# Performance work log

Hardware: AMD Instinct MI355X
Metric: run time of the kernel (lower is better)

Reference implementation:

```python
import jax, jax.numpy as jnp
import numpy as np

META_HIDDEN = 32


def _meta_apply(t, mw1, mb1, mw2, mb2):
    # t: [..., 3] triples; meta MLP 3 -> META_HIDDEN -> 1 (ReLU)
    h = jax.nn.relu(jnp.einsum('...k,hk->...h', t, mw1) + mb1)
    return jnp.einsum('...h,h->...', h, mw2[0]) + mb2[0]


def _meta_update_layer(v_in, w, v_out, mw1, mb1, mw2, mb2):
    # v_in: [I] (batch-0 input activations), w: [O, I], v_out: [O] (batch-0 output activations)
    # Builds the triples [v_i, w_ij, v_j] for every (i, j) pair and runs one batched meta pass.
    t = jnp.stack([
        jnp.broadcast_to(v_in[None, :], w.shape),
        w,
        jnp.broadcast_to(v_out[:, None], w.shape),
    ], axis=-1)  # [O, I, 3]
    return _meta_apply(t, mw1, mb1, mw2, mb2)  # [O, I] new weights


def setup_inputs() -> dict:
    key = jax.random.key(0)
    ks = jax.random.split(key, 12)
    I, H1, H2, O, B = 1024, 2048, 2048, 1024, 32
    def lin(kw, fan_in, fan_out):
        s = 1.0 / np.sqrt(fan_in)
        return jax.random.uniform(kw, (fan_out, fan_in), jnp.float32, -s, s)
    x = jax.random.normal(ks[0], (B, I), jnp.float32)
    w1 = lin(ks[1], I, H1); b1 = jax.random.uniform(ks[2], (H1,), jnp.float32, -1/np.sqrt(I), 1/np.sqrt(I))
    w2 = lin(ks[3], H1, H2); b2 = jax.random.uniform(ks[4], (H2,), jnp.float32, -1/np.sqrt(H1), 1/np.sqrt(H1))
    w3 = lin(ks[5], H2, O); b3 = jax.random.uniform(ks[6], (O,), jnp.float32, -1/np.sqrt(H2), 1/np.sqrt(H2))
    # meta network 3 -> META_HIDDEN -> 1
    mw1 = lin(ks[7], 3, META_HIDDEN); mb1 = jax.random.uniform(ks[8], (META_HIDDEN,), jnp.float32, -1/np.sqrt(3), 1/np.sqrt(3))
    mw2 = lin(ks[9], META_HIDDEN, 1); mb2 = jax.random.uniform(ks[10], (1,), jnp.float32, -1/np.sqrt(META_HIDDEN), 1/np.sqrt(META_HIDDEN))
    return {"x": x, "w1": w1, "b1": b1, "w2": w2, "b2": b2, "w3": w3, "b3": b3,
            "mw1": mw1, "mb1": mb1, "mw2": mw2, "mb2": mb2}


def reference(x, w1, b1, w2, b2, w3, b3, mw1, mb1, mw2, mb2):
    # Main 3-layer MLP forward (ReLU after every layer, including the last, as in the source).
    a0 = x
    a1 = jax.nn.relu(a0 @ w1.T + b1)
    a2 = jax.nn.relu(a1 @ w2.T + b2)
    out = jax.nn.relu(a2 @ w3.T + b3)
    # Per-weight meta update: original code loops over every (input, output) neuron pair of
    # each fc weight and writes meta_weight([v_i, w_ij, v_j]) back into the weight.
    # Only batch row 0 of the activations is used (impulse[i].data[0, idx]).
    nw1 = _meta_update_layer(a0[0], w1, a1[0], mw1, mb1, mw2, mb2)
    nw2 = _meta_update_layer(a1[0], w2, a2[0], mw1, mb1, mw2, mb2)
    nw3 = _meta_update_layer(a2[0], w3, out[0], mw1, mb1, mw2, mb2)
    return out, nw1, nw2, nw3
```

## Files before the change

kernel.cpp:

```cpp
#include <hip/hip_runtime.h>

#define NT 256

typedef float f2 __attribute__((ext_vector_type(2)));

__device__ __forceinline__ void meta_body(
    int g,
    const float* __restrict__ w1, const float* __restrict__ w2, const float* __restrict__ w3,
    const float* __restrict__ a0, const float* __restrict__ a1, const float* __restrict__ a2,
    const float* __restrict__ a3,
    float* __restrict__ n1, float* __restrict__ n2, float* __restrict__ n3,
    const float* __restrict__ mw1, const float* __restrict__ mb1,
    const float* __restrict__ mw2, const float* __restrict__ mb2) {
  const int n1c = (2048 * 1024) / 8;
  const int n2c = (2048 * 2048) / 8;

  const float* W; const float* vin; const float* vout; float* nw;
  int sh, e;
  if (g < n1c)            { W = w1; vin = a0; vout = a1; nw = n1; sh = 10; e = g; }
  else if (g < n1c + n2c) { W = w2; vin = a1; vout = a2; nw = n2; sh = 11; e = g - n1c; }
  else                    { W = w3; vin = a2; vout = a3; nw = n3; sh = 11; e = g - n1c - n2c; }

  const int base = e << 3;
  const int o = base >> sh;
  const int i0 = base & ((1 << sh) - 1);

  f2 wv[4], vv[4];
  {
    float4 t0 = *reinterpret_cast<const float4*>(&W[base]);
    float4 t1 = *reinterpret_cast<const float4*>(&W[base + 4]);
    wv[0] = (f2){t0.x, t0.y}; wv[1] = (f2){t0.z, t0.w};
    wv[2] = (f2){t1.x, t1.y}; wv[3] = (f2){t1.z, t1.w};
    float4 u0 = *reinterpret_cast<const float4*>(&vin[i0]);
    float4 u1 = *reinterpret_cast<const float4*>(&vin[i0 + 4]);
    vv[0] = (f2){u0.x, u0.y}; vv[1] = (f2){u0.z, u0.w};
    vv[2] = (f2){u1.x, u1.y}; vv[3] = (f2){u1.z, u1.w};
  }
  const float vo = vout[o];
  const float c2 = mb2[0];

  float r[32];
  #pragma unroll
  for (int j = 0; j < 32; ++j)
    r[j] = fmaf(mw1[3 * j + 2], vo, mb1[j]);

  f2 acc[4];
  #pragma unroll
  for (int p = 0; p < 4; ++p) acc[p] = (f2){c2, c2};

  const f2 zero = (f2){0.f, 0.f};
  #pragma unroll
  for (int j = 0; j < 32; ++j) {
    const float aj = mw1[3 * j];
    const float bj = mw1[3 * j + 1];
    const float mj = mw2[j];
    const f2 a2v = (f2){aj, aj};
    const f2 b2v = (f2){bj, bj};
    const f2 m2v = (f2){mj, mj};
    const f2 r2v = (f2){r[j], r[j]};
    #pragma unroll
    for (int p = 0; p < 4; ++p) {
#if __has_builtin(__builtin_elementwise_fma) && __has_builtin(__builtin_elementwise_max)
      f2 q = __builtin_elementwise_fma(a2v, vv[p], r2v);
      f2 h = __builtin_elementwise_fma(b2v, wv[p], q);
      h = __builtin_elementwise_max(h, zero);
      acc[p] = __builtin_elementwise_fma(m2v, h, acc[p]);
#else
      f2 h;
      h.x = fmaxf(fmaf(bj, wv[p].x, fmaf(aj, vv[p].x, r[j])), 0.f);
      h.y = fmaxf(fmaf(bj, wv[p].y, fmaf(aj, vv[p].y, r[j])), 0.f);
      acc[p].x = fmaf(mj, h.x, acc[p].x);
      acc[p].y = fmaf(mj, h.y, acc[p].y);
#endif
    }
  }

  float4 o0 = make_float4(acc[0].x, acc[0].y, acc[1].x, acc[1].y);
  float4 o1 = make_float4(acc[2].x, acc[2].y, acc[3].x, acc[3].y);
  *reinterpret_cast<float4*>(&nw[base])     = o0;
  *reinterpret_cast<float4*>(&nw[base + 4]) = o1;
}

template<int KL>
__device__ __forceinline__ void gemm_body(
    int gbid, const float* __restrict__ A, const float* __restrict__ W,
    float* __restrict__ P, int K, int O,
    float* __restrict__ Wt, float* __restrict__ At) {
  constexpr int NG = KL / 4;
  constexpr int PM = NG - 1;
  const int tid = threadIdx.x;
  const int ks = gbid & 31;
  const int obase = (gbid >> 5) << 7;
  const int kbeg = ks * KL;

  #pragma unroll
  for (int t = 0; t < (128 * NG) / NT; ++t) {
    const int s = tid + t * NT;
    const int r = s / NG, p = s % NG;
    const float4 v = *reinterpret_cast<const float4*>(
        &W[(size_t)(obase + r) * K + kbeg + 4 * p]);
    *reinterpret_cast<float4*>(&Wt[r * KL + 4 * (p ^ (r & PM))]) = v;
  }
  #pragma unroll
  for (int t = 0; t < (32 * NG + NT - 1) / NT; ++t) {
    const int s = tid + t * NT;
    if ((32 * NG) % NT == 0 || s < 32 * NG) {
      const int r = s / NG, p = s % NG;
      *reinterpret_cast<float4*>(&At[r * KL + 4 * p]) =
          *reinterpret_cast<const float4*>(&A[(size_t)r * K + kbeg + 4 * p]);
    }
  }
  __syncthreads();

  const int to = tid & 31;
  const int b0 = (tid >> 5) << 2;
  float acc[4][4];
  #pragma unroll
  for (int i = 0; i < 4; ++i)
    #pragma unroll
    for (int j = 0; j < 4; ++j) acc[i][j] = 0.f;

  #pragma unroll
  for (int gq = 0; gq < NG; ++gq) {
    float4 av[4], wv[4];
    #pragma unroll
    for (int j = 0; j < 4; ++j)
      av[j] = *reinterpret_cast<const float4*>(&At[(b0 + j) * KL + 4 * gq]);
    const int c = 4 * (gq ^ (to & PM));
    #pragma unroll
    for (int i = 0; i < 4; ++i)
      wv[i] = *reinterpret_cast<const float4*>(&Wt[(to + 32 * i) * KL + c]);
    #pragma unroll
    for (int i = 0; i < 4; ++i) {
      #pragma unroll
      for (int j = 0; j < 4; ++j) {
        acc[i][j] = fmaf(wv[i].x, av[j].x, acc[i][j]);
        acc[i][j] = fmaf(wv[i].y, av[j].y, acc[i][j]);
        acc[i][j] = fmaf(wv[i].z, av[j].z, acc[i][j]);
        acc[i][j] = fmaf(wv[i].w, av[j].w, acc[i][j]);
      }
    }
  }

  #pragma unroll
  for (int i = 0; i < 4; ++i)
    #pragma unroll
    for (int j = 0; j < 4; ++j)
      P[(size_t)(ks * 32 + b0 + j) * O + obase + to + 32 * i] = acc[i][j];
}

template<int KL>
__global__ __launch_bounds__(NT) void combo(
    int nGemm,
    const float* __restrict__ A, const float* __restrict__ W,
    float* __restrict__ P, int K, int O,
    int gbase,
    const float* __restrict__ w1, const float* __restrict__ w2, const float* __restrict__ w3,
    const float* __restrict__ a0, const float* __restrict__ a1, const float* __restrict__ a2,
    const float* __restrict__ a3,
    float* __restrict__ n1, float* __restrict__ n2, float* __restrict__ n3,
    const float* __restrict__ mw1, const float* __restrict__ mb1,
    const float* __restrict__ mw2, const float* __restrict__ mb2) {
  __shared__ float Wt[128 * KL];
  __shared__ float At[32 * KL];
  const int bid = blockIdx.x;
  if (bid < nGemm) {
    gemm_body<KL>(bid, A, W, P, K, O, Wt, At);
  } else {
    const int g = gbase + (bid - nGemm) * NT + threadIdx.x;
    meta_body(g, w1, w2, w3, a0, a1, a2, a3, n1, n2, n3, mw1, mb1, mw2, mb2);
  }
}

__global__ __launch_bounds__(NT) void meta_only(
    int gbase,
    const float* __restrict__ w1, const float* __restrict__ w2, const float* __restrict__ w3,
    const float* __restrict__ a0, const float* __restrict__ a1, const float* __restrict__ a2,
    const float* __restrict__ a3,
    float* __restrict__ n1, float* __restrict__ n2, float* __restrict__ n3,
    const float* __restrict__ mw1, const float* __restrict__ mb1,
    const float* __restrict__ mw2, const float* __restrict__ mb2) {
  const int g = gbase + blockIdx.x * NT + threadIdx.x;
  meta_body(g, w1, w2, w3, a0, a1, a2, a3, n1, n2, n3, mw1, mb1, mw2, mb2);
}

template<int OSH>
__global__ __launch_bounds__(NT) void red32(
    const float* __restrict__ P, const float* __restrict__ bias,
    float* __restrict__ C) {
  const int e = blockIdx.x * NT + threadIdx.x;
  const int o = e & ((1 << OSH) - 1);
  float s = 0.f;
  #pragma unroll
  for (int ks = 0; ks < 32; ++ks)
    s += P[((size_t)ks << (5 + OSH)) + e];
  C[e] = fmaxf(s + bias[o], 0.f);
}

extern "C" void kernel_launch(void* const* d_in, const int* in_sizes, int n_in,
                              void* d_out, int out_size, void* d_ws, size_t ws_size,
                              hipStream_t stream) {
  const float* x   = (const float*)d_in[0];
  const float* w1  = (const float*)d_in[1];
  const float* b1  = (const float*)d_in[2];
  const float* w2  = (const float*)d_in[3];
  const float* b2  = (const float*)d_in[4];
  const float* w3  = (const float*)d_in[5];
  const float* b3  = (const float*)d_in[6];
  const float* mw1 = (const float*)d_in[7];
  const float* mb1 = (const float*)d_in[8];
  const float* mw2 = (const float*)d_in[9];
  const float* mb2 = (const float*)d_in[10];

  float* out = (float*)d_out;
  float* n1  = out + 32 * 1024;
  float* n2  = n1 + 2048 * 1024;
  float* n3  = n2 + 2048 * 2048;

  float* ws = (float*)d_ws;
  float* a1 = ws;
  float* a2 = ws + 65536;
  float* P  = ws + 131072;

  combo<32><<<512, NT, 0, stream>>>(512, x, w1, P, 1024, 2048,
      0, w1, w2, w3, x, a1, a2, out, n1, n2, n3, mw1, mb1, mw2, mb2);
  red32<11><<<(32 * 2048) / NT, NT, 0, stream>>>(P, b1, a1);
  combo<64><<<512 + 1024, NT, 0, stream>>>(512, a1, w2, P, 2048, 2048,
      0, w1, w2, w3, x, a1, a2, out, n1, n2, n3, mw1, mb1, mw2, mb2);
  red32<11><<<(32 * 2048) / NT, NT, 0, stream>>>(P, b2, a2);
  combo<64><<<256 + 2048, NT, 0, stream>>>(256, a2, w3, P, 2048, 1024,
      262144, w1, w2, w3, x, a1, a2, out, n1, n2, n3, mw1, mb1, mw2, mb2);
  red32<10><<<(32 * 1024) / NT, NT, 0, stream>>>(P, b3, out);
  meta_only<<<1024, NT, 0, stream>>>(786432, w1, w2, w3, x, a1, a2, out,
                                     n1, n2, n3, mw1, mb1, mw2, mb2);
}
```

Before: 59.89 us.

## Transpose activations and compute GEMM split-K without shared memory

Replaces the shared-memory tiled split-K GEMM with a register-heavy scheme. Each thread owns one output neuron and accumulates all 32 batch rows over a K slice, reading activations stored transposed ([K][32]) so that loads are wave-uniform broadcasts. This adds a transpose kernel for x and reduction kernels that emit transposed activations plus a compact row-0 vector for the meta pass. The partial-sum buffer is moved into the n3 output region before that region is overwritten. The change removes LDS staging and barriers, at the cost of 32 accumulators per thread and strided per-thread weight reads.

```diff
diff --git a/kernel.cpp b/kernel.cpp
--- a/kernel.cpp
+++ b/kernel.cpp
@@ -3,6 +3,33 @@
 #define NT 256
 
 typedef float f2 __attribute__((ext_vector_type(2)));
+
+__global__ __launch_bounds__(NT) void transp_x(const float* __restrict__ x,
+                                               float* __restrict__ xT) {
+  __shared__ float T[64][33];
+  const int k0 = blockIdx.x * 64;
+  const int t = threadIdx.x;
+  {
+    const int s = t * 8;
+    const int b = s >> 6;
+    const int c = s & 63;
+    float4 v0 = *(const float4*)&x[b * 1024 + k0 + c];
+    float4 v1 = *(const float4*)&x[b * 1024 + k0 + c + 4];
+    T[c + 0][b] = v0.x; T[c + 1][b] = v0.y; T[c + 2][b] = v0.z; T[c + 3][b] = v0.w;
+    T[c + 4][b] = v1.x; T[c + 5][b] = v1.y; T[c + 6][b] = v1.z; T[c + 7][b] = v1.w;
+  }
+  __syncthreads();
+  {
+    const int s = t * 8;
+    const int r = s >> 5;
+    const int b0 = s & 31;
+    float o[8];
+    #pragma unroll
+    for (int q = 0; q < 8; ++q) o[q] = T[r][b0 + q];
+    *(float4*)&xT[(k0 + r) * 32 + b0]     = make_float4(o[0], o[1], o[2], o[3]);
+    *(float4*)&xT[(k0 + r) * 32 + b0 + 4] = make_float4(o[4], o[5], o[6], o[7]);
+  }
+}
 
 __device__ __forceinline__ void meta_body(
     int g,
@@ -75,84 +102,52 @@
     }
   }
 
-  float4 o0 = make_float4(acc[0].x, acc[0].y, acc[1].x, acc[1].y);
-  float4 o1 = make_float4(acc[2].x, acc[2].y, acc[3].x, acc[3].y);
-  *reinterpret_cast<float4*>(&nw[base])     = o0;
-  *reinterpret_cast<float4*>(&nw[base + 4]) = o1;
-}
-
-template<int KL>
+  *reinterpret_cast<float4*>(&nw[base])     = make_float4(acc[0].x, acc[0].y, acc[1].x, acc[1].y);
+  *reinterpret_cast<float4*>(&nw[base + 4]) = make_float4(acc[2].x, acc[2].y, acc[3].x, acc[3].y);
+}
+
+template<int KLW, int NTO_LOG>
 __device__ __forceinline__ void gemm_body(
-    int gbid, const float* __restrict__ A, const float* __restrict__ W,
-    float* __restrict__ P, int K, int O,
-    float* __restrict__ Wt, float* __restrict__ At) {
-  constexpr int NG = KL / 4;
-  constexpr int PM = NG - 1;
+    int gbid, const float* __restrict__ AT, const float* __restrict__ W,
+    float* __restrict__ P, int K, int O) {
   const int tid = threadIdx.x;
-  const int ks = gbid & 31;
-  const int obase = (gbid >> 5) << 7;
-  const int kbeg = ks * KL;
-
-  #pragma unroll
-  for (int t = 0; t < (128 * NG) / NT; ++t) {
-    const int s = tid + t * NT;
-    const int r = s / NG, p = s % NG;
-    const float4 v = *reinterpret_cast<const float4*>(
-        &W[(size_t)(obase + r) * K + kbeg + 4 * p]);
-    *reinterpret_cast<float4*>(&Wt[r * KL + 4 * (p ^ (r & PM))]) = v;
-  }
-  #pragma unroll
-  for (int t = 0; t < (32 * NG + NT - 1) / NT; ++t) {
-    const int s = tid + t * NT;
-    if ((32 * NG) % NT == 0 || s < 32 * NG) {
-      const int r = s / NG, p = s % NG;
-      *reinterpret_cast<float4*>(&At[r * KL + 4 * p]) =
-          *reinterpret_cast<const float4*>(&A[(size_t)r * K + kbeg + 4 * p]);
+  const int otile = gbid & ((1 << NTO_LOG) - 1);
+  const int ksx = gbid >> NTO_LOG;
+  const int ol = tid & 63;
+  const int o = (otile << 6) + ol;
+  const int slice = __builtin_amdgcn_readfirstlane(ksx * 4 + (tid >> 6));
+  const int kbeg = slice * KLW;
+
+  const float* __restrict__ wp = W + (size_t)o * K + kbeg;
+  const float* __restrict__ ap = AT + (size_t)kbeg * 32;
+
+  float acc[32];
+  #pragma unroll
+  for (int b = 0; b < 32; ++b) acc[b] = 0.f;
+
+  #pragma unroll 2
+  for (int kk = 0; kk < KLW; kk += 4) {
+    const float4 wv = *(const float4*)(wp + kk);
+    #pragma unroll
+    for (int q = 0; q < 4; ++q) {
+      const float wq = (q == 0) ? wv.x : (q == 1) ? wv.y : (q == 2) ? wv.z : wv.w;
+      #pragma unroll
+      for (int b = 0; b < 32; ++b)
+        acc[b] = fmaf(wq, ap[(kk + q) * 32 + b], acc[b]);
     }
   }
-  __syncthreads();
-
-  const int to = tid & 31;
-  const int b0 = (tid >> 5) << 2;
-  float acc[4][4];
-  #pragma unroll
-  for (int i = 0; i < 4; ++i)
-    #pragma unroll
-    for (int j = 0; j < 4; ++j) acc[i][j] = 0.f;
-
-  #pragma unroll
-  for (int gq = 0; gq < NG; ++gq) {
-    float4 av[4], wv[4];
-    #pragma unroll
-    for (int j = 0; j < 4; ++j)
-      av[j] = *reinterpret_cast<const float4*>(&At[(b0 + j) * KL + 4 * gq]);
-    const int c = 4 * (gq ^ (to & PM));
-    #pragma unroll
-    for (int i = 0; i < 4; ++i)
-      wv[i] = *reinterpret_cast<const float4*>(&Wt[(to + 32 * i) * KL + c]);
-    #pragma unroll
-    for (int i = 0; i < 4; ++i) {
-      #pragma unroll
-      for (int j = 0; j < 4; ++j) {
-        acc[i][j] = fmaf(wv[i].x, av[j].x, acc[i][j]);
-        acc[i][j] = fmaf(wv[i].y, av[j].y, acc[i][j]);
-        acc[i][j] = fmaf(wv[i].z, av[j].z, acc[i][j]);
-        acc[i][j] = fmaf(wv[i].w, av[j].w, acc[i][j]);
-      }
-    }
-  }
-
-  #pragma unroll
-  for (int i = 0; i < 4; ++i)
-    #pragma unroll
-    for (int j = 0; j < 4; ++j)
-      P[(size_t)(ks * 32 + b0 + j) * O + obase + to + 32 * i] = acc[i][j];
-}
-
-template<int KL>
-__global__ __launch_bounds__(NT) void combo(
+
+  float* pp = P + ((size_t)slice * O + o) * 32;
+  #pragma unroll
+  for (int c = 0; c < 8; ++c)
+    *(float4*)(pp + c * 4) =
+        make_float4(acc[c * 4], acc[c * 4 + 1], acc[c * 4 + 2], acc[c * 4 + 3]);
+}
+
+template<int KLW, int NTO_LOG>
+__global__ __launch_bounds__(NT) void gemm_meta(
     int nGemm,
-    const float* __restrict__ A, const float* __restrict__ W,
+    const float* __restrict__ AT, const float* __restrict__ W,
     float* __restrict__ P, int K, int O,
     int gbase,
     const float* __restrict__ w1, const float* __restrict__ w2, const float* __restrict__ w3,
@@ -161,11 +156,9 @@
     float* __restrict__ n1, float* __restrict__ n2, float* __restrict__ n3,
     const float* __restrict__ mw1, const float* __restrict__ mb1,
     const float* __restrict__ mw2, const float* __restrict__ mb2) {
-  __shared__ float Wt[128 * KL];
-  __shared__ float At[32 * KL];
   const int bid = blockIdx.x;
   if (bid < nGemm) {
-    gemm_body<KL>(bid, A, W, P, K, O, Wt, At);
+    gemm_body<KLW, NTO_LOG>(bid, AT, W, P, K, O);
   } else {
     const int g = gbase + (bid - nGemm) * NT + threadIdx.x;
     meta_body(g, w1, w2, w3, a0, a1, a2, a3, n1, n2, n3, mw1, mb1, mw2, mb2);
@@ -184,17 +177,43 @@
   meta_body(g, w1, w2, w3, a0, a1, a2, a3, n1, n2, n3, mw1, mb1, mw2, mb2);
 }
 
-template<int OSH>
-__global__ __launch_bounds__(NT) void red32(
+template<int NS, int NTO_LOG>
+__global__ __launch_bounds__(NT) void reduceT(
     const float* __restrict__ P, const float* __restrict__ bias,
-    float* __restrict__ C) {
-  const int e = blockIdx.x * NT + threadIdx.x;
-  const int o = e & ((1 << OSH) - 1);
+    float* __restrict__ aT, float* __restrict__ row0, int O) {
+  const int otile = blockIdx.x & ((1 << NTO_LOG) - 1);
+  const int part = blockIdx.x >> NTO_LOG;
+  const int local = part * NT + threadIdx.x;
+  const int o = (otile << 6) + (local >> 5);
+  const int b = local & 31;
   float s = 0.f;
   #pragma unroll
-  for (int ks = 0; ks < 32; ++ks)
-    s += P[((size_t)ks << (5 + OSH)) + e];
-  C[e] = fmaxf(s + bias[o], 0.f);
+  for (int sl = 0; sl < NS; ++sl)
+    s += P[((size_t)sl * O + o) * 32 + b];
+  const float v = fmaxf(s + bias[o], 0.f);
+  aT[o * 32 + b] = v;
+  if (b == 0) row0[o] = v;
+}
+
+template<int NS>
+__global__ __launch_bounds__(NT) void reduceOut(
+    const float* __restrict__ P, const float* __restrict__ bias,
+    float* __restrict__ out, int O) {
+  __shared__ float T[8][33];
+  const int otile = blockIdx.x & 15;
+  const int part = blockIdx.x >> 4;
+  const int local = part * NT + threadIdx.x;
+  const int o = (otile << 6) + (local >> 5);
+  const int b = local & 31;
+  float s = 0.f;
+  #pragma unroll
+  for (int sl = 0; sl < NS; ++sl)
+    s += P[((size_t)sl * O + o) * 32 + b];
+  T[(local >> 5) & 7][b] = fmaxf(s + bias[o], 0.f);
+  __syncthreads();
+  const int b2 = threadIdx.x >> 3;
+  const int oo = threadIdx.x & 7;
+  out[b2 * O + (otile << 6) + (part << 3) + oo] = T[oo][b2];
 }
 
 extern "C" void kernel_launch(void* const* d_in, const int* in_sizes, int n_in,
@@ -216,21 +235,25 @@
   float* n1  = out + 32 * 1024;
   float* n2  = n1 + 2048 * 1024;
   float* n3  = n2 + 2048 * 2048;
-
-  float* ws = (float*)d_ws;
-  float* a1 = ws;
-  float* a2 = ws + 65536;
-  float* P  = ws + 131072;
-
-  combo<32><<<512, NT, 0, stream>>>(512, x, w1, P, 1024, 2048,
-      0, w1, w2, w3, x, a1, a2, out, n1, n2, n3, mw1, mb1, mw2, mb2);
-  red32<11><<<(32 * 2048) / NT, NT, 0, stream>>>(P, b1, a1);
-  combo<64><<<512 + 1024, NT, 0, stream>>>(512, a1, w2, P, 2048, 2048,
-      0, w1, w2, w3, x, a1, a2, out, n1, n2, n3, mw1, mb1, mw2, mb2);
-  red32<11><<<(32 * 2048) / NT, NT, 0, stream>>>(P, b2, a2);
-  combo<64><<<256 + 2048, NT, 0, stream>>>(256, a2, w3, P, 2048, 1024,
-      262144, w1, w2, w3, x, a1, a2, out, n1, n2, n3, mw1, mb1, mw2, mb2);
-  red32<10><<<(32 * 1024) / NT, NT, 0, stream>>>(P, b3, out);
-  meta_only<<<1024, NT, 0, stream>>>(786432, w1, w2, w3, x, a1, a2, out,
+  float* P   = n3;
+
+  float* ws  = (float*)d_ws;
+  float* xT  = ws;
+  float* a1T = ws + 32768;
+  float* a2T = a1T + 65536;
+  float* v1  = a2T + 65536;
+  float* v2  = v1 + 2048;
+
+  transp_x<<<16, NT, 0, stream>>>(x, xT);
+  gemm_meta<32, 5><<<256, NT, 0, stream>>>(256, xT, w1, P, 1024, 2048,
+      0, w1, w2, w3, x, v1, v2, out, n1, n2, n3, mw1, mb1, mw2, mb2);
+  reduceT<32, 5><<<256, NT, 0, stream>>>(P, b1, a1T, v1, 2048);
+  gemm_meta<64, 5><<<256 + 1024, NT, 0, stream>>>(256, a1T, w2, P, 2048, 2048,
+      0, w1, w2, w3, x, v1, v2, out, n1, n2, n3, mw1, mb1, mw2, mb2);
+  reduceT<32, 5><<<256, NT, 0, stream>>>(P, b2, a2T, v2, 2048);
+  gemm_meta<32, 4><<<256 + 2048, NT, 0, stream>>>(256, a2T, w3, P, 2048, 1024,
+      262144, w1, w2, w3, x, v1, v2, out, n1, n2, n3, mw1, mb1, mw2, mb2);
+  reduceOut<64><<<128, NT, 0, stream>>>(P, b3, out, 1024);
+  meta_only<<<1024, NT, 0, stream>>>(786432, w1, w2, w3, x, v1, v2, out,
                                      n1, n2, n3, mw1, mb1, mw2, mb2);
 }
```

Result: slower. 81.02 us (+35.3%).
